# Kernel optimization log

Measured on AMD Instinct MI355X. Metric: run time of the kernel, lower is better.

Reference implementation:

```python
import jax, jax.numpy as jnp
import numpy as np

B, L, D = 2, 2048, 1024
DH = 64
NH = D // DH
EPS = 1e-5
NEG = -1e30


def rms_norm(x, w):
    # x: (..., dh); norm in fp32 like the torch module, then scale by weight
    xf = x.astype(jnp.float32)
    y = xf * jax.lax.rsqrt(jnp.mean(xf * xf, axis=-1, keepdims=True) + EPS)
    return y.astype(x.dtype) * w.astype(x.dtype)


def sdpa(q, k, v, m):
    # q:(b,h,lq,dh) k,v:(b,h,lk,dh) m:(lq,lk) bool
    scale = 1.0 / jnp.sqrt(jnp.asarray(DH, q.dtype))
    s = jnp.einsum('bhqd,bhkd->bhqk', q, k) * scale
    s = jnp.where(m[None, None], s, NEG)
    p = jax.nn.softmax(s, axis=-1)
    return jnp.einsum('bhqk,bhkd->bhqd', p, v)


def setup_inputs() -> dict:
    key = jax.random.key(0)
    k1, k2, k3 = jax.random.split(key, 3)
    x = jax.random.normal(k1, (B, L, D), dtype=jnp.float32)
    mask = jnp.tril(jnp.ones((L, L), dtype=bool))  # causal: no fully-masked rows
    w_qkv = jax.random.normal(k2, (3 * D, D), dtype=jnp.float32) * (1.0 / np.sqrt(D))
    w_fc = jax.random.normal(k3, (D, D), dtype=jnp.float32) * (1.0 / np.sqrt(D))
    q_norm_w = jnp.ones((DH,), dtype=jnp.float32)
    k_norm_w = jnp.ones((DH,), dtype=jnp.float32)
    return {"x": x, "mask": mask, "w_qkv": w_qkv, "w_fc": w_fc,
            "q_norm_w": q_norm_w, "k_norm_w": k_norm_w,
            "subset_attention_size": 1024}


def reference(x, mask, w_qkv, w_fc, q_norm_w, k_norm_w, subset_attention_size):
    b, l, d = x.shape
    qkv = jnp.einsum('bld,ed->ble', x, w_qkv)  # (b,l,3d)
    q, k, v = jnp.split(qkv, 3, axis=-1)

    def heads(t):
        return t.reshape(b, l, NH, DH).transpose(0, 2, 1, 3)  # (b,nh,l,dh)

    q, k, v = heads(q), heads(k), heads(v)
    q = rms_norm(q, q_norm_w)
    k = rms_norm(k, k_norm_w)

    S = subset_attention_size
    if S is not None and S < l:
        o1 = sdpa(q[:, :, :S], k[:, :, :S], v[:, :, :S], mask[:S, :S])
        o2 = sdpa(q[:, :, S:], k, v, mask[S:, :])
        o = jnp.concatenate([o1, o2], axis=2)
    else:
        o = sdpa(q, k, v, mask)
    o = o.transpose(0, 2, 1, 3).reshape(b, l, d)  # (b,l,d)
    return jnp.einsum('bld,ed->ble', o, w_fc)
```

## Files before the change

kernel.cpp:

```cpp
#include <hip/hip_runtime.h>

typedef __bf16 bf16x8 __attribute__((ext_vector_type(8)));
typedef __bf16 bf16x4 __attribute__((ext_vector_type(4)));
typedef float f32x4 __attribute__((ext_vector_type(4)));
typedef short s16x4 __attribute__((ext_vector_type(4)));
typedef unsigned short u16;
typedef unsigned int u32;
typedef unsigned short u16x4 __attribute__((ext_vector_type(4)));
typedef unsigned short u16x8 __attribute__((ext_vector_type(8)));

#define AS1 __attribute__((address_space(1)))
#define AS3 __attribute__((address_space(3)))

__device__ __forceinline__ u16 f2bf(float f) {
  unsigned u = __builtin_bit_cast(unsigned, f);
  u += 0x7fffu + ((u >> 16) & 1u);
  return (u16)(u >> 16);
}

__device__ __forceinline__ f32x4 mfma16(s16x4 a, s16x4 b, f32x4 c) {
#if __has_builtin(__builtin_amdgcn_mfma_f32_16x16x16bf16_1k)
  return __builtin_amdgcn_mfma_f32_16x16x16bf16_1k(a, b, c, 0, 0, 0);
#else
  asm("v_mfma_f32_16x16x16_bf16 %0, %1, %2, %0" : "+v"(c) : "v"(a), "v"(b));
  return c;
#endif
}

__global__ __launch_bounds__(256) void cvt_all(const float* __restrict__ x,
                                               const float* __restrict__ wq,
                                               const float* __restrict__ wf,
                                               u16* __restrict__ xb, u16* __restrict__ wqb,
                                               u16* __restrict__ wfb) {
  long i = ((long)blockIdx.x * 256 + threadIdx.x) * 4;
  const float* src;
  u16* dst;
  long off;
  if (i < 4194304L) {
    src = x; dst = xb; off = i;
  } else if (i < 7340032L) {
    src = wq; dst = wqb; off = i - 4194304L;
  } else {
    src = wf; dst = wfb; off = i - 7340032L;
  }
  float4 v = *reinterpret_cast<const float4*>(src + off);
  u16x4 o;
  o.x = f2bf(v.x); o.y = f2bf(v.y); o.z = f2bf(v.z); o.w = f2bf(v.w);
  *reinterpret_cast<u16x4*>(dst + off) = o;
}

__global__ __launch_bounds__(256, 2) void gemm_qkv(const u16* __restrict__ A,
                                                   const u16* __restrict__ W,
                                                   u16* __restrict__ C,
                                                   const float* __restrict__ qw,
                                                   const float* __restrict__ kw) {
  constexpr int N = 3072, K = 1024;
  __shared__ __align__(16) u16 As[128 * 32];
  __shared__ __align__(16) u16 Bs[128 * 32];
  const int tid = threadIdx.x;
  const int lane = tid & 63;
  const int wid = tid >> 6;
  const int wm = wid >> 1, wn = wid & 1;
  const int l16 = lane & 15, g4 = lane >> 4;
  const long bm = blockIdx.x, bn = blockIdx.y;

  const int srow = tid >> 2;
  const int scol = (tid & 3) * 8;
  const u16* aA0 = A + (bm * 128 + srow) * (long)K + scol;
  const u16* aA1 = aA0 + 64 * (long)K;
  const u16* aW0 = W + (bn * 128 + srow) * (long)K + scol;
  const u16* aW1 = aW0 + 64 * (long)K;

  f32x4 acc[4][4] = {};

  for (int kt = 0; kt < K; kt += 32) {
    __builtin_amdgcn_global_load_lds((AS1 void*)(aA0 + kt), (AS3 void*)(&As[tid * 8]), 16, 0, 0);
    __builtin_amdgcn_global_load_lds((AS1 void*)(aA1 + kt), (AS3 void*)(&As[2048 + tid * 8]), 16, 0, 0);
    __builtin_amdgcn_global_load_lds((AS1 void*)(aW0 + kt), (AS3 void*)(&Bs[tid * 8]), 16, 0, 0);
    __builtin_amdgcn_global_load_lds((AS1 void*)(aW1 + kt), (AS3 void*)(&Bs[2048 + tid * 8]), 16, 0, 0);
    __syncthreads();
    bf16x8 af[4], bfr[4];
#pragma unroll
    for (int m = 0; m < 4; ++m)
      af[m] = *reinterpret_cast<const bf16x8*>(&As[(wm * 64 + m * 16 + l16) * 32 + g4 * 8]);
#pragma unroll
    for (int n = 0; n < 4; ++n)
      bfr[n] = *reinterpret_cast<const bf16x8*>(&Bs[(wn * 64 + n * 16 + l16) * 32 + g4 * 8]);
#pragma unroll
    for (int m = 0; m < 4; ++m)
#pragma unroll
      for (int n = 0; n < 4; ++n)
        acc[m][n] = __builtin_amdgcn_mfma_f32_16x16x32_bf16(af[m], bfr[n], acc[m][n], 0, 0, 0);
    __syncthreads();
  }

  if (bn < 16) {
    const float qscale = 0.18033688011112042f;
    const float* w = (bn < 8) ? qw : kw;
    const float ws = (bn < 8) ? qscale : 1.0f;
    float wv[4];
#pragma unroll
    for (int n = 0; n < 4; ++n) wv[n] = w[n * 16 + l16] * ws;
#pragma unroll
    for (int m = 0; m < 4; ++m) {
#pragma unroll
      for (int j = 0; j < 4; ++j) {
        float ss = 0.f;
#pragma unroll
        for (int n = 0; n < 4; ++n) ss = fmaf(acc[m][n][j], acc[m][n][j], ss);
        ss += __shfl_xor(ss, 1);
        ss += __shfl_xor(ss, 2);
        ss += __shfl_xor(ss, 4);
        ss += __shfl_xor(ss, 8);
        const float inv = rsqrtf(ss * (1.0f / 64.0f) + 1e-5f);
#pragma unroll
        for (int n = 0; n < 4; ++n) acc[m][n][j] *= inv * wv[n];
      }
    }
  }

#pragma unroll
  for (int m = 0; m < 4; ++m)
#pragma unroll
    for (int n = 0; n < 4; ++n)
#pragma unroll
      for (int j = 0; j < 4; ++j) {
        long row = bm * 128 + wm * 64 + m * 16 + g4 * 4 + j;
        long col = bn * 128 + wn * 64 + n * 16 + l16;
        C[row * N + col] = f2bf(acc[m][n][j]);
      }
}

__global__ __launch_bounds__(256, 2) void gemm_fc(const u16* __restrict__ A,
                                                  const u16* __restrict__ W,
                                                  float* __restrict__ C) {
  constexpr int N = 1024, K = 1024;
  __shared__ __align__(16) u16 As[128 * 32];
  __shared__ __align__(16) u16 Bs[64 * 32];
  const int tid = threadIdx.x;
  const int lane = tid & 63;
  const int wid = tid >> 6;
  const int wm = wid >> 1, wn = wid & 1;
  const int l16 = lane & 15, g4 = lane >> 4;
  const long bm = blockIdx.x, bn = blockIdx.y;

  const int srow = tid >> 2;
  const int scol = (tid & 3) * 8;
  const u16* aA0 = A + (bm * 128 + srow) * (long)K + scol;
  const u16* aA1 = aA0 + 64 * (long)K;
  const u16* aW0 = W + (bn * 64 + srow) * (long)K + scol;

  f32x4 acc[4][2] = {};

  for (int kt = 0; kt < K; kt += 32) {
    __builtin_amdgcn_global_load_lds((AS1 void*)(aA0 + kt), (AS3 void*)(&As[tid * 8]), 16, 0, 0);
    __builtin_amdgcn_global_load_lds((AS1 void*)(aA1 + kt), (AS3 void*)(&As[2048 + tid * 8]), 16, 0, 0);
    __builtin_amdgcn_global_load_lds((AS1 void*)(aW0 + kt), (AS3 void*)(&Bs[tid * 8]), 16, 0, 0);
    __syncthreads();
    bf16x8 af[4], bfr[2];
#pragma unroll
    for (int m = 0; m < 4; ++m)
      af[m] = *reinterpret_cast<const bf16x8*>(&As[(wm * 64 + m * 16 + l16) * 32 + g4 * 8]);
#pragma unroll
    for (int n = 0; n < 2; ++n)
      bfr[n] = *reinterpret_cast<const bf16x8*>(&Bs[(wn * 32 + n * 16 + l16) * 32 + g4 * 8]);
#pragma unroll
    for (int m = 0; m < 4; ++m)
#pragma unroll
      for (int n = 0; n < 2; ++n)
        acc[m][n] = __builtin_amdgcn_mfma_f32_16x16x32_bf16(af[m], bfr[n], acc[m][n], 0, 0, 0);
    __syncthreads();
  }

#pragma unroll
  for (int m = 0; m < 4; ++m)
#pragma unroll
    for (int n = 0; n < 2; ++n)
#pragma unroll
      for (int j = 0; j < 4; ++j) {
        long row = bm * 128 + wm * 64 + m * 16 + g4 * 4 + j;
        long col = bn * 64 + wn * 32 + n * 16 + l16;
        C[row * N + col] = acc[m][n][j];
      }
}

__global__ __launch_bounds__(256) void vtrans(const u16* __restrict__ qkv,
                                              u16* __restrict__ vt) {
  __shared__ u16 T[64][66];
  const int tid = threadIdx.x;
  const int f = blockIdx.x;
  const int bh = (f & 7) * 4 + (f >> 8);
  const int ktile = (f >> 3) & 31;
  const long vbase = (long)(bh >> 4) * 2048 * 3072 + (bh & 15) * 64 + 2048;
  const int r = tid >> 2, c = (tid & 3) * 16;
  const u16* src = qkv + vbase + (long)(ktile * 64 + r) * 3072 + c;
  *reinterpret_cast<u16x8*>(&T[r][c]) = *reinterpret_cast<const u16x8*>(src);
  *reinterpret_cast<u16x8*>(&T[r][c + 8]) = *reinterpret_cast<const u16x8*>(src + 8);
  __syncthreads();
  const int dr = tid >> 2, kc = (tid & 3) * 16;
  u16 buf[16];
#pragma unroll
  for (int j = 0; j < 16; ++j) buf[j] = T[kc + j][dr];
  u16* dst = vt + (long)bh * 131072 + (long)dr * 2048 + ktile * 64 + kc;
  *reinterpret_cast<u16x8*>(dst) = *reinterpret_cast<u16x8*>(&buf[0]);
  *reinterpret_cast<u16x8*>(dst + 8) = *reinterpret_cast<u16x8*>(&buf[8]);
}

__global__ __launch_bounds__(256, 4) void attn_causal(const u16* __restrict__ qkv,
                                                      const u16* __restrict__ vt,
                                                      u16* __restrict__ o) {
  __shared__ __align__(16) u16 SMEM[16384];

  const int tid = threadIdx.x, lane = tid & 63, wid = tid >> 6;
  const int l16 = lane & 15, g4 = lane >> 4;
  const int h8 = (l16 & 7) << 4;
  const int qh = wid & 1, kh = wid >> 1;

  const int f = blockIdx.x;
  const int xcd = f & 7;
  const int g = f >> 3;
  const int hb = g >> 5;
  const int w = g & 31;
  const int bh = xcd * 4 + hb;
  const int basei = (w & 1) ? (31 - (w >> 1)) : (w >> 1);
  const int it = (hb & 1) ? (31 - basei) : basei;

  const long base = (long)(bh >> 4) * 2048 * 3072 + (bh & 15) * 64;
  const u16* qb = qkv + base;
  const u16* kb = qkv + base + 1024;
  const u16* vtb = vt + (long)bh * 131072;

  bf16x8 qv[2][2];
#pragma unroll
  for (int qf = 0; qf < 2; ++qf) {
    const u16* qp = qb + ((long)it * 64 + qh * 32 + qf * 16 + l16) * 3072;
    qv[qf][0] = *reinterpret_cast<const bf16x8*>(qp + g4 * 8);
    qv[qf][1] = *reinterpret_cast<const bf16x8*>(qp + 32 + g4 * 8);
  }

  f32x4 acc[2][4] = {};
  f32x4 lacc[2] = {};

  s16x4 ones4;
#pragma unroll
  for (int j = 0; j < 4; ++j) ones4[j] = (short)0x3F80;

  const int krow = tid >> 3;
  const int scolE = (((tid & 7) * 16) ^ ((krow & 7) << 4)) >> 1;

  auto stage_issue = [&](int buf, int kt) {
    u16* KB = SMEM + buf * 4096;
    u16* VB = SMEM + 8192 + buf * 4096;
    __builtin_amdgcn_global_load_lds((AS1 void*)(kb + (long)(kt * 64 + krow) * 3072 + scolE),
                                     (AS3 void*)(&KB[tid * 8]), 16, 0, 0);
    __builtin_amdgcn_global_load_lds((AS1 void*)(kb + (long)(kt * 64 + krow + 32) * 3072 + scolE),
                                     (AS3 void*)(&KB[2048 + tid * 8]), 16, 0, 0);
    __builtin_amdgcn_global_load_lds((AS1 void*)(vtb + (long)krow * 2048 + kt * 64 + scolE),
                                     (AS3 void*)(&VB[tid * 8]), 16, 0, 0);
    __builtin_amdgcn_global_load_lds((AS1 void*)(vtb + (long)(krow + 32) * 2048 + kt * 64 + scolE),
                                     (AS3 void*)(&VB[2048 + tid * 8]), 16, 0, 0);
  };

  auto tile_step = [&](int cur, bool diag) {
    if (diag && qh == 0 && kh == 1) return;
    const u16* KB = SMEM + cur * 4096;
    const u16* VB = SMEM + 8192 + cur * 4096;
    bf16x8 kfr[2][2];
#pragma unroll
    for (int kf = 0; kf < 2; ++kf) {
      const int row = kh * 32 + kf * 16 + l16;
#pragma unroll
      for (int ck = 0; ck < 2; ++ck)
        kfr[kf][ck] = *reinterpret_cast<const bf16x8*>(
            &KB[row * 64 + (((ck * 64 + g4 * 16) ^ h8) >> 1)]);
    }
    f32x4 s[2][2];
    __builtin_amdgcn_s_setprio(1);
#pragma unroll
    for (int kf = 0; kf < 2; ++kf)
#pragma unroll
      for (int qf = 0; qf < 2; ++qf) {
        f32x4 z = {0.f, 0.f, 0.f, 0.f};
        z = __builtin_amdgcn_mfma_f32_16x16x32_bf16(kfr[kf][0], qv[qf][0], z, 0, 0, 0);
        z = __builtin_amdgcn_mfma_f32_16x16x32_bf16(kfr[kf][1], qv[qf][1], z, 0, 0, 0);
        s[kf][qf] = z;
      }
    __builtin_amdgcn_s_setprio(0);
    if (diag) {
#pragma unroll
      for (int kf = 0; kf < 2; ++kf)
#pragma unroll
        for (int qf = 0; qf < 2; ++qf) {
          const int keyl = kh * 32 + kf * 16 + g4 * 4;
          const int ql = qh * 32 + qf * 16 + l16;
#pragma unroll
          for (int j = 0; j < 4; ++j)
            if (keyl + j > ql) s[kf][qf][j] = -3e38f;
        }
    }
    s16x4 pfr[2][2];
#pragma unroll
    for (int kf = 0; kf < 2; ++kf)
#pragma unroll
      for (int qf = 0; qf < 2; ++qf) {
        bf16x4 p;
#pragma unroll
        for (int j = 0; j < 4; ++j) p[j] = (__bf16)exp2f(s[kf][qf][j]);
        pfr[kf][qf] = __builtin_bit_cast(s16x4, p);
      }
    __builtin_amdgcn_s_setprio(1);
#pragma unroll
    for (int qf = 0; qf < 2; ++qf) {
      lacc[qf] = mfma16(pfr[0][qf], ones4, lacc[qf]);
      lacc[qf] = mfma16(pfr[1][qf], ones4, lacc[qf]);
    }
#pragma unroll
    for (int db = 0; db < 4; ++db) {
      const int vrow = db * 16 + l16;
#pragma unroll
      for (int kf = 0; kf < 2; ++kf) {
        const u16x4 vv = *reinterpret_cast<const u16x4*>(
            &VB[vrow * 64 + (((kh * 64 + kf * 32 + g4 * 8) ^ h8) >> 1)]);
        const s16x4 vf = __builtin_bit_cast(s16x4, vv);
#pragma unroll
        for (int qf = 0; qf < 2; ++qf) acc[qf][db] = mfma16(pfr[kf][qf], vf, acc[qf][db]);
      }
    }
    __builtin_amdgcn_s_setprio(0);
  };

  stage_issue(0, 0);
  __syncthreads();

  for (int kt = 0; kt < it; ++kt) {
    const int cur = kt & 1;
    stage_issue(cur ^ 1, kt + 1);
    tile_step(cur, false);
    __syncthreads();
  }
  tile_step(it & 1, true);
  __syncthreads();

  float* Ebuf = reinterpret_cast<float*>(SMEM);
  const int ebase = qh * 2176;
  if (kh == 1) {
#pragma unroll
    for (int qf = 0; qf < 2; ++qf) {
#pragma unroll
      for (int db = 0; db < 4; ++db)
#pragma unroll
        for (int j = 0; j < 4; ++j)
          Ebuf[ebase + (qf * 16 + g4 * 4 + j) * 68 + db * 16 + l16] = acc[qf][db][j];
      if (l16 == 0) {
#pragma unroll
        for (int j = 0; j < 4; ++j)
          Ebuf[ebase + (qf * 16 + g4 * 4 + j) * 68 + 64] = lacc[qf][j];
      }
    }
  }
  __syncthreads();
  if (kh == 0) {
    const long obase = (long)(bh >> 4) * 2048 * 1024 + (bh & 15) * 64;
#pragma unroll
    for (int qf = 0; qf < 2; ++qf) {
      float linv[4];
#pragma unroll
      for (int j = 0; j < 4; ++j) {
        const float lsum = lacc[qf][j] + Ebuf[ebase + (qf * 16 + g4 * 4 + j) * 68 + 64];
        linv[j] = 1.0f / lsum;
      }
#pragma unroll
      for (int db = 0; db < 4; ++db)
#pragma unroll
        for (int j = 0; j < 4; ++j) {
          const int row = qh * 32 + qf * 16 + g4 * 4 + j;
          const float v =
              acc[qf][db][j] + Ebuf[ebase + (qf * 16 + g4 * 4 + j) * 68 + db * 16 + l16];
          o[obase + ((long)it * 64 + row) * 1024 + db * 16 + l16] = f2bf(v * linv[j]);
        }
    }
  }
}

extern "C" void kernel_launch(void* const* d_in, const int* in_sizes, int n_in,
                              void* d_out, int out_size, void* d_ws, size_t ws_size,
                              hipStream_t stream) {
  const float* x = (const float*)d_in[0];
  const float* w_qkv = (const float*)d_in[2];
  const float* w_fc = (const float*)d_in[3];
  const float* qw = (const float*)d_in[4];
  const float* kw = (const float*)d_in[5];
  float* out = (float*)d_out;

  char* ws = (char*)d_ws;
  u16* xb    = (u16*)(ws);
  u16* wqkvb = (u16*)(ws + (8L << 20));
  u16* wfcb  = (u16*)(ws + (14L << 20));
  u16* qkv   = (u16*)(ws + (16L << 20));
  u16* ob    = (u16*)(ws + (40L << 20));
  u16* vt    = xb;

  cvt_all<<<8192, 256, 0, stream>>>(x, w_qkv, w_fc, xb, wqkvb, wfcb);
  gemm_qkv<<<dim3(32, 24), 256, 0, stream>>>(xb, wqkvb, qkv, qw, kw);
  vtrans<<<1024, 256, 0, stream>>>(qkv, vt);
  attn_causal<<<1024, 256, 0, stream>>>(qkv, vt, ob);
  gemm_fc<<<dim3(32, 16), 256, 0, stream>>>(ob, wfcb, out);
}
```

Before: 108.9 us.

## Enlarge attention query tile to 128 rows with 8 waves per block

```diff
diff --git a/kernel.cpp b/kernel.cpp
--- a/kernel.cpp
+++ b/kernel.cpp
@@ -206,24 +206,26 @@
   *reinterpret_cast<u16x8*>(dst + 8) = *reinterpret_cast<u16x8*>(&buf[8]);
 }
 
-__global__ __launch_bounds__(256, 4) void attn_causal(const u16* __restrict__ qkv,
+__global__ __launch_bounds__(512, 4) void attn_causal(const u16* __restrict__ qkv,
                                                       const u16* __restrict__ vt,
                                                       u16* __restrict__ o) {
   __shared__ __align__(16) u16 SMEM[16384];
+  __shared__ __align__(16) float Ebuf[4][32][68];
 
   const int tid = threadIdx.x, lane = tid & 63, wid = tid >> 6;
   const int l16 = lane & 15, g4 = lane >> 4;
   const int h8 = (l16 & 7) << 4;
-  const int qh = wid & 1, kh = wid >> 1;
+  const int qh = wid & 3, kh = wid >> 2;
 
   const int f = blockIdx.x;
   const int xcd = f & 7;
   const int g = f >> 3;
-  const int hb = g >> 5;
-  const int w = g & 31;
+  const int hb = g >> 4;
+  const int w = g & 15;
   const int bh = xcd * 4 + hb;
-  const int basei = (w & 1) ? (31 - (w >> 1)) : (w >> 1);
-  const int it = (hb & 1) ? (31 - basei) : basei;
+  const int basei = (w & 1) ? (15 - (w >> 1)) : (w >> 1);
+  const int refl = (hb ^ (hb >> 1)) & 1;
+  const int it = refl ? (15 - basei) : basei;
 
   const long base = (long)(bh >> 4) * 2048 * 3072 + (bh & 15) * 64;
   const u16* qb = qkv + base;
@@ -233,7 +235,7 @@
   bf16x8 qv[2][2];
 #pragma unroll
   for (int qf = 0; qf < 2; ++qf) {
-    const u16* qp = qb + ((long)it * 64 + qh * 32 + qf * 16 + l16) * 3072;
+    const u16* qp = qb + ((long)it * 128 + qh * 32 + qf * 16 + l16) * 3072;
     qv[qf][0] = *reinterpret_cast<const bf16x8*>(qp + g4 * 8);
     qv[qf][1] = *reinterpret_cast<const bf16x8*>(qp + 32 + g4 * 8);
   }
@@ -253,16 +255,15 @@
     u16* VB = SMEM + 8192 + buf * 4096;
     __builtin_amdgcn_global_load_lds((AS1 void*)(kb + (long)(kt * 64 + krow) * 3072 + scolE),
                                      (AS3 void*)(&KB[tid * 8]), 16, 0, 0);
-    __builtin_amdgcn_global_load_lds((AS1 void*)(kb + (long)(kt * 64 + krow + 32) * 3072 + scolE),
-                                     (AS3 void*)(&KB[2048 + tid * 8]), 16, 0, 0);
     __builtin_amdgcn_global_load_lds((AS1 void*)(vtb + (long)krow * 2048 + kt * 64 + scolE),
                                      (AS3 void*)(&VB[tid * 8]), 16, 0, 0);
-    __builtin_amdgcn_global_load_lds((AS1 void*)(vtb + (long)(krow + 32) * 2048 + kt * 64 + scolE),
-                                     (AS3 void*)(&VB[2048 + tid * 8]), 16, 0, 0);
   };
 
-  auto tile_step = [&](int cur, bool diag) {
-    if (diag && qh == 0 && kh == 1) return;
+  auto tile_step = [&](int cur, int kt) {
+    const int qb0 = it * 128 + qh * 32;
+    const int kb0 = kt * 64 + kh * 32;
+    if (kb0 > qb0 + 31) return;
+    const bool needMask = (kb0 + 31) > qb0;
     const u16* KB = SMEM + cur * 4096;
     const u16* VB = SMEM + 8192 + cur * 4096;
     bf16x8 kfr[2][2];
@@ -286,13 +287,13 @@
         s[kf][qf] = z;
       }
     __builtin_amdgcn_s_setprio(0);
-    if (diag) {
+    if (needMask) {
 #pragma unroll
       for (int kf = 0; kf < 2; ++kf)
 #pragma unroll
         for (int qf = 0; qf < 2; ++qf) {
-          const int keyl = kh * 32 + kf * 16 + g4 * 4;
-          const int ql = qh * 32 + qf * 16 + l16;
+          const int keyl = kb0 + kf * 16 + g4 * 4;
+          const int ql = qb0 + qf * 16 + l16;
 #pragma unroll
           for (int j = 0; j < 4; ++j)
             if (keyl + j > ql) s[kf][qf][j] = -3e38f;
@@ -332,17 +333,16 @@
   stage_issue(0, 0);
   __syncthreads();
 
-  for (int kt = 0; kt < it; ++kt) {
+  const int ktend = 2 * it + 1;
+  for (int kt = 0; kt < ktend; ++kt) {
     const int cur = kt & 1;
     stage_issue(cur ^ 1, kt + 1);
-    tile_step(cur, false);
+    tile_step(cur, kt);
     __syncthreads();
   }
-  tile_step(it & 1, true);
+  tile_step(ktend & 1, ktend);
   __syncthreads();
 
-  float* Ebuf = reinterpret_cast<float*>(SMEM);
-  const int ebase = qh * 2176;
   if (kh == 1) {
 #pragma unroll
     for (int qf = 0; qf < 2; ++qf) {
@@ -350,11 +350,10 @@
       for (int db = 0; db < 4; ++db)
 #pragma unroll
         for (int j = 0; j < 4; ++j)
-          Ebuf[ebase + (qf * 16 + g4 * 4 + j) * 68 + db * 16 + l16] = acc[qf][db][j];
+          Ebuf[qh][qf * 16 + g4 * 4 + j][db * 16 + l16] = acc[qf][db][j];
       if (l16 == 0) {
 #pragma unroll
-        for (int j = 0; j < 4; ++j)
-          Ebuf[ebase + (qf * 16 + g4 * 4 + j) * 68 + 64] = lacc[qf][j];
+        for (int j = 0; j < 4; ++j) Ebuf[qh][qf * 16 + g4 * 4 + j][64] = lacc[qf][j];
       }
     }
   }
@@ -366,7 +365,7 @@
       float linv[4];
 #pragma unroll
       for (int j = 0; j < 4; ++j) {
-        const float lsum = lacc[qf][j] + Ebuf[ebase + (qf * 16 + g4 * 4 + j) * 68 + 64];
+        const float lsum = lacc[qf][j] + Ebuf[qh][qf * 16 + g4 * 4 + j][64];
         linv[j] = 1.0f / lsum;
       }
 #pragma unroll
@@ -374,9 +373,8 @@
 #pragma unroll
         for (int j = 0; j < 4; ++j) {
           const int row = qh * 32 + qf * 16 + g4 * 4 + j;
-          const float v =
-              acc[qf][db][j] + Ebuf[ebase + (qf * 16 + g4 * 4 + j) * 68 + db * 16 + l16];
-          o[obase + ((long)it * 64 + row) * 1024 + db * 16 + l16] = f2bf(v * linv[j]);
+          const float v = acc[qf][db][j] + Ebuf[qh][qf * 16 + g4 * 4 + j][db * 16 + l16];
+          o[obase + ((long)it * 128 + row) * 1024 + db * 16 + l16] = f2bf(v * linv[j]);
         }
     }
   }
@@ -403,6 +401,6 @@
   cvt_all<<<8192, 256, 0, stream>>>(x, w_qkv, w_fc, xb, wqkvb, wfcb);
   gemm_qkv<<<dim3(32, 24), 256, 0, stream>>>(xb, wqkvb, qkv, qw, kw);
   vtrans<<<1024, 256, 0, stream>>>(qkv, vt);
-  attn_causal<<<1024, 256, 0, stream>>>(qkv, vt, ob);
+  attn_causal<<<512, 512, 0, stream>>>(qkv, vt, ob);
   gemm_fc<<<dim3(32, 16), 256, 0, stream>>>(ob, wfcb, out);
 }
```

Result: slower. 115.5 us (+6.0%).

## Fuse V transpose into QKV GEMM epilogue and split Q/K buffers

Applied to the files above, without the earlier changes.

```diff
diff --git a/kernel.cpp b/kernel.cpp
--- a/kernel.cpp
+++ b/kernel.cpp
@@ -51,12 +51,15 @@
 
 __global__ __launch_bounds__(256, 2) void gemm_qkv(const u16* __restrict__ A,
                                                    const u16* __restrict__ W,
-                                                   u16* __restrict__ C,
+                                                   u16* __restrict__ Qb,
+                                                   u16* __restrict__ Kbf,
+                                                   u16* __restrict__ vt,
                                                    const float* __restrict__ qw,
                                                    const float* __restrict__ kw) {
-  constexpr int N = 3072, K = 1024;
+  constexpr int K = 1024;
   __shared__ __align__(16) u16 As[128 * 32];
   __shared__ __align__(16) u16 Bs[128 * 32];
+  __shared__ __align__(16) u16 Ts[128 * 136];
   const int tid = threadIdx.x;
   const int lane = tid & 63;
   const int wid = tid >> 6;
@@ -117,18 +120,48 @@
         for (int n = 0; n < 4; ++n) acc[m][n][j] *= inv * wv[n];
       }
     }
-  }
-
-#pragma unroll
-  for (int m = 0; m < 4; ++m)
-#pragma unroll
-    for (int n = 0; n < 4; ++n)
-#pragma unroll
-      for (int j = 0; j < 4; ++j) {
-        long row = bm * 128 + wm * 64 + m * 16 + g4 * 4 + j;
-        long col = bn * 128 + wn * 64 + n * 16 + l16;
-        C[row * N + col] = f2bf(acc[m][n][j]);
-      }
+    u16* dst = (bn < 8) ? Qb : Kbf;
+    const long cb = (bn < 8) ? bn : (bn - 8);
+#pragma unroll
+    for (int m = 0; m < 4; ++m)
+#pragma unroll
+      for (int n = 0; n < 4; ++n)
+#pragma unroll
+        for (int j = 0; j < 4; ++j) {
+          long row = bm * 128 + wm * 64 + m * 16 + g4 * 4 + j;
+          long col = cb * 128 + wn * 64 + n * 16 + l16;
+          dst[row * 1024 + col] = f2bf(acc[m][n][j]);
+        }
+  } else {
+#pragma unroll
+    for (int m = 0; m < 4; ++m)
+#pragma unroll
+      for (int n = 0; n < 4; ++n) {
+        bf16x4 w4;
+#pragma unroll
+        for (int j = 0; j < 4; ++j) w4[j] = (__bf16)acc[m][n][j];
+        const int lc = wn * 64 + n * 16 + l16;
+        const int lr = wm * 64 + m * 16 + g4 * 4;
+        *reinterpret_cast<bf16x4*>(&Ts[lc * 136 + lr]) = w4;
+      }
+    __syncthreads();
+    const int b = (int)(bm >> 4);
+    const int keybase = ((int)(bm & 15)) * 128;
+#pragma unroll
+    for (int u = 0; u < 2; ++u) {
+      const int unit = u * 256 + tid;
+      const int hh = unit >> 8;
+      const int d = (unit >> 2) & 63;
+      const int kc = (unit & 3) * 32;
+      const long bhv = b * 16 + (bn - 16) * 2 + hh;
+      u16* dstp = vt + bhv * 131072L + (long)d * 2048 + keybase + kc;
+      const u16* srcp = &Ts[(hh * 64 + d) * 136 + kc];
+#pragma unroll
+      for (int c = 0; c < 4; ++c)
+        *reinterpret_cast<u16x8*>(dstp + c * 8) =
+            *reinterpret_cast<const u16x8*>(srcp + c * 8);
+    }
+  }
 }
 
 __global__ __launch_bounds__(256, 2) void gemm_fc(const u16* __restrict__ A,
@@ -184,29 +217,8 @@
       }
 }
 
-__global__ __launch_bounds__(256) void vtrans(const u16* __restrict__ qkv,
-                                              u16* __restrict__ vt) {
-  __shared__ u16 T[64][66];
-  const int tid = threadIdx.x;
-  const int f = blockIdx.x;
-  const int bh = (f & 7) * 4 + (f >> 8);
-  const int ktile = (f >> 3) & 31;
-  const long vbase = (long)(bh >> 4) * 2048 * 3072 + (bh & 15) * 64 + 2048;
-  const int r = tid >> 2, c = (tid & 3) * 16;
-  const u16* src = qkv + vbase + (long)(ktile * 64 + r) * 3072 + c;
-  *reinterpret_cast<u16x8*>(&T[r][c]) = *reinterpret_cast<const u16x8*>(src);
-  *reinterpret_cast<u16x8*>(&T[r][c + 8]) = *reinterpret_cast<const u16x8*>(src + 8);
-  __syncthreads();
-  const int dr = tid >> 2, kc = (tid & 3) * 16;
-  u16 buf[16];
-#pragma unroll
-  for (int j = 0; j < 16; ++j) buf[j] = T[kc + j][dr];
-  u16* dst = vt + (long)bh * 131072 + (long)dr * 2048 + ktile * 64 + kc;
-  *reinterpret_cast<u16x8*>(dst) = *reinterpret_cast<u16x8*>(&buf[0]);
-  *reinterpret_cast<u16x8*>(dst + 8) = *reinterpret_cast<u16x8*>(&buf[8]);
-}
-
-__global__ __launch_bounds__(256, 4) void attn_causal(const u16* __restrict__ qkv,
+__global__ __launch_bounds__(256, 4) void attn_causal(const u16* __restrict__ Qb,
+                                                      const u16* __restrict__ Kbf,
                                                       const u16* __restrict__ vt,
                                                       u16* __restrict__ o) {
   __shared__ __align__(16) u16 SMEM[16384];
@@ -225,15 +237,15 @@
   const int basei = (w & 1) ? (31 - (w >> 1)) : (w >> 1);
   const int it = (hb & 1) ? (31 - basei) : basei;
 
-  const long base = (long)(bh >> 4) * 2048 * 3072 + (bh & 15) * 64;
-  const u16* qb = qkv + base;
-  const u16* kb = qkv + base + 1024;
+  const long base = (long)(bh >> 4) * 2048 * 1024 + (bh & 15) * 64;
+  const u16* qb = Qb + base;
+  const u16* kb = Kbf + base;
   const u16* vtb = vt + (long)bh * 131072;
 
   bf16x8 qv[2][2];
 #pragma unroll
   for (int qf = 0; qf < 2; ++qf) {
-    const u16* qp = qb + ((long)it * 64 + qh * 32 + qf * 16 + l16) * 3072;
+    const u16* qp = qb + ((long)it * 64 + qh * 32 + qf * 16 + l16) * 1024;
     qv[qf][0] = *reinterpret_cast<const bf16x8*>(qp + g4 * 8);
     qv[qf][1] = *reinterpret_cast<const bf16x8*>(qp + 32 + g4 * 8);
   }
@@ -251,9 +263,9 @@
   auto stage_issue = [&](int buf, int kt) {
     u16* KB = SMEM + buf * 4096;
     u16* VB = SMEM + 8192 + buf * 4096;
-    __builtin_amdgcn_global_load_lds((AS1 void*)(kb + (long)(kt * 64 + krow) * 3072 + scolE),
+    __builtin_amdgcn_global_load_lds((AS1 void*)(kb + (long)(kt * 64 + krow) * 1024 + scolE),
                                      (AS3 void*)(&KB[tid * 8]), 16, 0, 0);
-    __builtin_amdgcn_global_load_lds((AS1 void*)(kb + (long)(kt * 64 + krow + 32) * 3072 + scolE),
+    __builtin_amdgcn_global_load_lds((AS1 void*)(kb + (long)(kt * 64 + krow + 32) * 1024 + scolE),
                                      (AS3 void*)(&KB[2048 + tid * 8]), 16, 0, 0);
     __builtin_amdgcn_global_load_lds((AS1 void*)(vtb + (long)krow * 2048 + kt * 64 + scolE),
                                      (AS3 void*)(&VB[tid * 8]), 16, 0, 0);
@@ -396,13 +408,13 @@
   u16* xb    = (u16*)(ws);
   u16* wqkvb = (u16*)(ws + (8L << 20));
   u16* wfcb  = (u16*)(ws + (14L << 20));
-  u16* qkv   = (u16*)(ws + (16L << 20));
+  u16* Qb    = (u16*)(ws + (16L << 20));
+  u16* Kbf   = (u16*)(ws + (24L << 20));
+  u16* vt    = (u16*)(ws + (32L << 20));
   u16* ob    = (u16*)(ws + (40L << 20));
-  u16* vt    = xb;
 
   cvt_all<<<8192, 256, 0, stream>>>(x, w_qkv, w_fc, xb, wqkvb, wfcb);
-  gemm_qkv<<<dim3(32, 24), 256, 0, stream>>>(xb, wqkvb, qkv, qw, kw);
-  vtrans<<<1024, 256, 0, stream>>>(qkv, vt);
-  attn_causal<<<1024, 256, 0, stream>>>(qkv, vt, ob);
+  gemm_qkv<<<dim3(32, 24), 256, 0, stream>>>(xb, wqkvb, Qb, Kbf, vt, qw, kw);
+  attn_causal<<<1024, 256, 0, stream>>>(Qb, Kbf, vt, ob);
   gemm_fc<<<dim3(32, 16), 256, 0, stream>>>(ob, wfcb, out);
 }
```

Result: faster. 104.6 us (-4.0%).
